# Performance work log

Measured on AMD Instinct MI355X. Metric: run time of the kernel, lower is better.

Reference implementation:

```python
import jax, jax.numpy as jnp
import numpy as np

N_NODES = 50000
N_EDGES = 1600000
IN_SIZE = 128
HIDDEN = 128
OUT_SIZE = 64
NUM_LAYERS = 3
BN_EPS = 1e-5
GIN_EPS_INIT = 1e-5


def setup_inputs() -> dict:
    key = jax.random.key(0)
    ks = jax.random.split(key, 16)
    node_feat = jax.random.normal(ks[0], (N_NODES, IN_SIZE), dtype=jnp.float32)
    src = jax.random.randint(ks[1], (N_EDGES,), 0, N_NODES)
    dst = jax.random.randint(ks[2], (N_EDGES,), 0, N_NODES)
    # per-layer MLP params (in_size == hidden, so shapes are uniform across layers)
    s1 = 1.0 / np.sqrt(IN_SIZE)
    s2 = 1.0 / np.sqrt(HIDDEN)
    W1 = jax.random.uniform(ks[3], (NUM_LAYERS, IN_SIZE, HIDDEN), jnp.float32, -s1, s1)
    b1 = jax.random.uniform(ks[4], (NUM_LAYERS, HIDDEN), jnp.float32, -s1, s1)
    gamma = jnp.ones((NUM_LAYERS, HIDDEN), jnp.float32)
    beta = jnp.zeros((NUM_LAYERS, HIDDEN), jnp.float32)
    W2 = jax.random.uniform(ks[5], (NUM_LAYERS, HIDDEN, HIDDEN), jnp.float32, -s2, s2)
    b2 = jax.random.uniform(ks[6], (NUM_LAYERS, HIDDEN), jnp.float32, -s2, s2)
    eps = jnp.full((NUM_LAYERS,), GIN_EPS_INIT, jnp.float32)  # learnable GIN eps
    Wout = jax.random.uniform(ks[7], (HIDDEN, OUT_SIZE), jnp.float32, -s2, s2)
    bout = jax.random.uniform(ks[8], (OUT_SIZE,), jnp.float32, -s2, s2)
    return {"node_feat": node_feat, "src": src, "dst": dst,
            "W1": W1, "b1": b1, "gamma": gamma, "beta": beta,
            "W2": W2, "b2": b2, "eps": eps, "Wout": Wout, "bout": bout}


def reference(node_feat, src, dst, W1, b1, gamma, beta, W2, b2, eps, Wout, bout):
    n = node_feat.shape[0]
    h = node_feat
    for i in range(NUM_LAYERS):
        # sum-aggregate source features onto destination nodes
        agg = jax.ops.segment_sum(h[src], dst, num_segments=n)  # [N, d]
        x = (1.0 + eps[i]) * h + agg
        x = x @ W1[i] + b1[i]
        # BatchNorm1d (training mode: batch statistics, biased variance)
        mu = jnp.mean(x, axis=0)
        var = jnp.var(x, axis=0)
        x = (x - mu) * jax.lax.rsqrt(var + BN_EPS) * gamma[i] + beta[i]
        x = jax.nn.relu(x)
        h = jax.nn.relu(x @ W2[i] + b2[i])
    return h @ Wout + bout
```

## Files before the change

kernel.cpp:

```cpp
#include <hip/hip_runtime.h>

#define NN 50000
#define NE 1600000
#define HID 128
#define NB 196
#define BCAP 12288
#define SLH (NN * 32)

typedef _Float16 half8 __attribute__((ext_vector_type(8)));
typedef float floatx4 __attribute__((ext_vector_type(4)));
typedef unsigned int uintx4 __attribute__((ext_vector_type(4)));

__device__ __forceinline__ void mix_acc(float a[8], half8 t) {
  uintx4 u = __builtin_bit_cast(uintx4, t);
#pragma unroll
  for (int k = 0; k < 4; ++k) {
    asm("v_fma_mix_f32 %0, %1, %2, %0 op_sel:[0,0,0] op_sel_hi:[1,0,0]"
        : "+v"(a[2 * k]) : "v"(u[k]), "v"(1.0f));
    asm("v_fma_mix_f32 %0, %1, %2, %0 op_sel:[1,0,0] op_sel_hi:[1,0,0]"
        : "+v"(a[2 * k + 1]) : "v"(u[k]), "v"(1.0f));
  }
}


#define CVT_BLK 3125
#define CNT_BLK 391

__device__ __forceinline__ void pack_one(const float* __restrict__ W1,
                                         const float* __restrict__ W2,
                                         const float* __restrict__ Wout,
                                         _Float16* __restrict__ wp, int y, int t) {
  const float* W;
  _Float16* dstp;
  int NCT;
  if (y < 3) { W = W1 + (size_t)y * 16384; dstp = wp + y * 16384; NCT = 8; }
  else if (y < 6) { W = W2 + (size_t)(y - 3) * 16384; dstp = wp + 49152 + (y - 3) * 16384; NCT = 8; }
  else { W = Wout; dstp = wp + 98304; NCT = 4; }
  if (t >= 4 * NCT * 64) return;
  int lane = t & 63;
  int ct = (t >> 6) % NCT;
  int kb = t / (64 * NCT);
  int n = ct * 16 + (lane & 15);
  int k0 = kb * 32 + (lane >> 4) * 8;
  int N = NCT * 16;
#pragma unroll
  for (int j = 0; j < 8; ++j) dstp[t * 8 + j] = (_Float16)W[(k0 + j) * N + n];
}

__global__ __launch_bounds__(256) void k_prep(
    const float* __restrict__ nf, _Float16* __restrict__ hb,
    const float* __restrict__ W1, const float* __restrict__ W2,
    const float* __restrict__ Wout, _Float16* __restrict__ wp,
    const int* __restrict__ dst, int* __restrict__ gcnt) {
  const int b = blockIdx.x;
  const int tid = threadIdx.x;
  if (b < CVT_BLK) {
    int t = b * 256 + tid;
    const float4* x4 = (const float4*)nf;
    float4 u = x4[t * 2], v = x4[t * 2 + 1];
    half8 o;
    o[0] = (_Float16)u.x; o[1] = (_Float16)u.y; o[2] = (_Float16)u.z; o[3] = (_Float16)u.w;
    o[4] = (_Float16)v.x; o[5] = (_Float16)v.y; o[6] = (_Float16)v.z; o[7] = (_Float16)v.w;
    int node = t >> 4, c = t & 15;
    ((half8*)hb)[(size_t)(c >> 2) * (NN * 4) + node * 4 + (c & 3)] = o;
  } else if (b < CVT_BLK + CNT_BLK) {
    __shared__ int cnt[NB];
    for (int i = tid; i < NB; i += 256) cnt[i] = 0;
    __syncthreads();
    int base = (b - CVT_BLK) * 4096;
    for (int i = 0; i < 16; ++i) {
      int e = base + i * 256 + tid;
      if (e < NE) atomicAdd(&cnt[dst[e] >> 8], 1);
    }
    __syncthreads();
    for (int i = tid; i < NB; i += 256)
      if (cnt[i]) atomicAdd(&gcnt[i], cnt[i]);
  } else {
    int bb = b - (CVT_BLK + CNT_BLK);
    pack_one(W1, W2, Wout, wp, bb >> 3, ((bb & 7) << 8) | tid);
  }
}


__global__ __launch_bounds__(256) void kb_basescan(const int* __restrict__ gcnt,
                                                   int* __restrict__ bbase,
                                                   int* __restrict__ bcur) {
  __shared__ int s[256];
  int tid = threadIdx.x;
  int v = (tid < NB) ? gcnt[tid] : 0;
  s[tid] = v;
  __syncthreads();
  for (int d = 1; d < 256; d <<= 1) {
    int t = (tid >= d) ? s[tid - d] : 0;
    __syncthreads();
    s[tid] += t;
    __syncthreads();
  }
  int incl = s[tid];
  if (tid < NB) {
    bbase[tid] = incl - v;
    bcur[tid] = incl - v;
  }
  if (tid == NB - 1) bbase[NB] = incl;
}

__global__ __launch_bounds__(256) void kb_partition(const int* __restrict__ src,
                                                    const int* __restrict__ dst,
                                                    int* __restrict__ bcur,
                                                    int* __restrict__ ebuf, int E) {
  __shared__ int cnt[NB];
  __shared__ int sbase[NB];
  int tid = threadIdx.x;
  for (int i = tid; i < NB; i += 256) cnt[i] = 0;
  __syncthreads();
  int base = blockIdx.x * 4096;
  int myd[16], mys[16];
#pragma unroll
  for (int i = 0; i < 16; ++i) {
    int e = base + i * 256 + tid;
    if (e < E) {
      myd[i] = dst[e];
      mys[i] = src[e];
      atomicAdd(&cnt[myd[i] >> 8], 1);
    } else {
      myd[i] = -1;
    }
  }
  __syncthreads();
  for (int i = tid; i < NB; i += 256)
    sbase[i] = cnt[i] ? atomicAdd(&bcur[i], cnt[i]) : 0;
  __syncthreads();
  for (int i = tid; i < NB; i += 256) cnt[i] = 0;
  __syncthreads();
#pragma unroll
  for (int i = 0; i < 16; ++i) {
    if (myd[i] >= 0) {
      int b = myd[i] >> 8;
      int r = atomicAdd(&cnt[b], 1);
      ebuf[sbase[b] + r] = (mys[i] << 8) | (myd[i] & 255);
    }
  }
}

__global__ __launch_bounds__(256) void kb_csr(const int* __restrict__ ebuf,
                                              const int* __restrict__ bbase,
                                              int* __restrict__ rs,
                                              unsigned short* __restrict__ eidx, int M) {
  __shared__ int cnt[256];
  __shared__ int off[256];
  __shared__ int sbuf[BCAP];
  int tid = threadIdx.x;
  int b = blockIdx.x;
  int lo = bbase[b], hi = bbase[b + 1];
  int n = hi - lo;
  cnt[tid] = 0;
  __syncthreads();
  for (int i = tid; i < n; i += 256) atomicAdd(&cnt[ebuf[lo + i] & 255], 1);
  __syncthreads();
  int v = cnt[tid];
  off[tid] = v;
  __syncthreads();
  for (int d = 1; d < 256; d <<= 1) {
    int t = (tid >= d) ? off[tid - d] : 0;
    __syncthreads();
    off[tid] += t;
    __syncthreads();
  }
  int excl = off[tid] - v;
  int gnode = b * 256 + tid;
  if (gnode < M) rs[gnode] = lo + excl;
  if (b == NB - 1 && tid == 0) rs[M] = bbase[NB];
  __syncthreads();
  cnt[tid] = excl;
  __syncthreads();
  if (n <= BCAP) {
    for (int i = tid; i < n; i += 256) {
      int ed = ebuf[lo + i];
      int r = atomicAdd(&cnt[ed & 255], 1);
      sbuf[r] = ed >> 8;
    }
    __syncthreads();
    for (int i = tid; i < n; i += 256) eidx[lo + i] = (unsigned short)sbuf[i];
  } else {
    for (int i = tid; i < n; i += 256) {
      int ed = ebuf[lo + i];
      int r = atomicAdd(&cnt[ed & 255], 1);
      eidx[lo + r] = (unsigned short)(ed >> 8);
    }
  }
}


__global__ __launch_bounds__(512, 8) void k_agg(
    const int* __restrict__ rs, const unsigned short* __restrict__ eidx,
    const float* __restrict__ eps, int layer, const _Float16* __restrict__ h,
    _Float16* __restrict__ x) {
  const int tid = threadIdx.x;
  const int b = blockIdx.x;
  const int slice = (b & 7) >> 1;
  const int tile = ((b >> 3) << 1) | (b & 1);
  const int lane = tid & 63;
  const int wid = tid >> 6;
  const int sub = lane & 3;
  const int slot = (lane >> 2) & 3;
  const int ng = lane >> 4;
  const int node = tile * 32 + wid * 4 + ng;
  const char* hbase = (const char*)(h + (size_t)slice * SLH);
  const unsigned subsh = (unsigned)sub << 4;

  float a[8] = {0.f, 0.f, 0.f, 0.f, 0.f, 0.f, 0.f, 0.f};
  int e0 = 0, e1 = 0;
  if (node < NN) {
    e0 = rs[node];
    e1 = rs[node + 1];
  }
  int e = e0 + slot;
  for (; e + 12 < e1; e += 16) {
    unsigned s0 = eidx[e];
    unsigned s1 = eidx[e + 4];
    unsigned s2 = eidx[e + 8];
    unsigned s3 = eidx[e + 12];
    half8 v0 = *(const half8*)(hbase + ((s0 << 6) | subsh));
    half8 v1 = *(const half8*)(hbase + ((s1 << 6) | subsh));
    half8 v2 = *(const half8*)(hbase + ((s2 << 6) | subsh));
    half8 v3 = *(const half8*)(hbase + ((s3 << 6) | subsh));
    half8 t01 = v0 + v1;
    half8 t23 = v2 + v3;
    mix_acc(a, t01);
    mix_acc(a, t23);
  }
  if (e + 4 < e1) {
    unsigned s0 = eidx[e];
    unsigned s1 = eidx[e + 4];
    half8 v0 = *(const half8*)(hbase + ((s0 << 6) | subsh));
    half8 v1 = *(const half8*)(hbase + ((s1 << 6) | subsh));
    half8 t01 = v0 + v1;
    mix_acc(a, t01);
    e += 8;
  }
  for (; e < e1; e += 4) {
    unsigned s0 = eidx[e];
    half8 v = *(const half8*)(hbase + ((s0 << 6) | subsh));
    mix_acc(a, v);
  }
#pragma unroll
  for (int j = 0; j < 8; ++j) {
    a[j] += __shfl_xor(a[j], 4);
    a[j] += __shfl_xor(a[j], 8);
  }
  if (slot == 0 && node < NN) {
    const float ep = 1.0f + eps[layer];
    half8 hv = *(const half8*)(hbase + (((unsigned)node << 6) | subsh));
    half8 o;
#pragma unroll
    for (int j = 0; j < 8; ++j) o[j] = (_Float16)fmaf(ep, (float)hv[j], a[j]);
    *(half8*)(x + (size_t)node * 128 + slice * 32 + sub * 8) = o;
  }
}


__global__ __launch_bounds__(1024, 8) void k_gemm1(
    const _Float16* __restrict__ wp1, const float* __restrict__ b1L,
    float* __restrict__ csum, float* __restrict__ csq, _Float16* x) {
  __shared__ _Float16 As[64 * 136];
  __shared__ float sredS[512];
  __shared__ float sredQ[512];
  const int tid = threadIdx.x;
  const int wid = tid >> 6;
  const int lane = tid & 63;
  const int slot = lane >> 4;
  const int c8 = lane & 15;
  const int c8t = tid & 15;
  const int rowBase = blockIdx.x * 64;

  {
    int row = tid >> 4;
    int gr = rowBase + row;
    half8 v = {0, 0, 0, 0, 0, 0, 0, 0};
    if (gr < NN) v = *(const half8*)(x + (size_t)gr * 128 + c8t * 8);
    *(half8*)(As + row * 136 + c8t * 8) = v;
  }
  __syncthreads();

  const int rg = wid & 3;
  const int cg = wid >> 2;
  floatx4 acc[2];
  acc[0] = (floatx4){0.f, 0.f, 0.f, 0.f};
  acc[1] = (floatx4){0.f, 0.f, 0.f, 0.f};
  const half8* wp8 = (const half8*)wp1;
#pragma unroll
  for (int kb = 0; kb < 4; ++kb) {
    half8 a = *(const half8*)(As + (rg * 16 + c8) * 136 + kb * 32 + slot * 8);
#pragma unroll
    for (int t = 0; t < 2; ++t) {
      int ct = cg * 2 + t;
      acc[t] = __builtin_amdgcn_mfma_f32_16x16x32_f16(a, wp8[(kb * 8 + ct) * 64 + lane],
                                                      acc[t], 0, 0, 0);
    }
  }
  __syncthreads();

#pragma unroll
  for (int t = 0; t < 2; ++t) {
    int ct = cg * 2 + t;
    float bv = b1L[ct * 16 + c8];
    float ps = 0.f, pq = 0.f;
#pragma unroll
    for (int reg = 0; reg < 4; ++reg) {
      int row = rg * 16 + slot * 4 + reg;
      float xv = acc[t][reg] + bv;
      As[row * 136 + ct * 16 + c8] = (_Float16)xv;
      if (rowBase + row < NN) {
        ps += xv;
        pq += xv * xv;
      }
    }
    ps += __shfl_xor(ps, 16);
    ps += __shfl_xor(ps, 32);
    pq += __shfl_xor(pq, 16);
    pq += __shfl_xor(pq, 32);
    if (lane < 16) {
      sredS[wid * 32 + t * 16 + lane] = ps;
      sredQ[wid * 32 + t * 16 + lane] = pq;
    }
  }
  __syncthreads();

  {
    int row = tid >> 4;
    int gr = rowBase + row;
    if (gr < NN) {
      half8 v = *(half8*)(As + row * 136 + c8t * 8);
      *(half8*)(x + (size_t)gr * 128 + c8t * 8) = v;
    }
  }
  if (tid < 128) {
    int c = tid;
    int wbase = (c >> 5) * 4;
    int loc = c & 31;
    float s = sredS[wbase * 32 + loc] + sredS[(wbase + 1) * 32 + loc] +
              sredS[(wbase + 2) * 32 + loc] + sredS[(wbase + 3) * 32 + loc];
    atomicAdd(&csum[c], s);
  } else if (tid < 256) {
    int c = tid - 128;
    int wbase = (c >> 5) * 4;
    int loc = c & 31;
    float q = sredQ[wbase * 32 + loc] + sredQ[(wbase + 1) * 32 + loc] +
              sredQ[(wbase + 2) * 32 + loc] + sredQ[(wbase + 3) * 32 + loc];
    atomicAdd(&csq[c], q);
  }
}


template <int FINAL>
__global__ __launch_bounds__(1024, 8) void k_bn_gemm2(
    const _Float16* __restrict__ x, const _Float16* __restrict__ wp2,
    const float* __restrict__ b2L, const float* __restrict__ gammaL,
    const float* __restrict__ betaL, const float* __restrict__ csum,
    const float* __restrict__ csq, _Float16* __restrict__ hout,
    const _Float16* __restrict__ wpo, const float* __restrict__ boutp,
    float* __restrict__ out) {
  __shared__ _Float16 As[64 * 136];
  const int tid = threadIdx.x;
  const int wid = tid >> 6;
  const int lane = tid & 63;
  const int slot = lane >> 4;
  const int c8 = lane & 15;
  const int c8t = tid & 15;
  const int rowBase = blockIdx.x * 64;

  float sc[8], sh[8];
  {
    const float invM = 1.0f / (float)NN;
#pragma unroll
    for (int j = 0; j < 8; ++j) {
      int k = c8t * 8 + j;
      float mu = csum[k] * invM;
      float var = csq[k] * invM - mu * mu;
      float g = gammaL[k] * rsqrtf(var + 1e-5f);
      sc[j] = g;
      sh[j] = fmaf(-mu, g, betaL[k]);
    }
  }
  {
    int row = tid >> 4;
    int gr = rowBase + row;
    half8 v = {0, 0, 0, 0, 0, 0, 0, 0};
    if (gr < NN) {
      v = *(const half8*)(x + (size_t)gr * 128 + c8t * 8);
#pragma unroll
      for (int j = 0; j < 8; ++j)
        v[j] = (_Float16)fmaxf(fmaf((float)v[j], sc[j], sh[j]), 0.f);
    }
    *(half8*)(As + row * 136 + c8t * 8) = v;
  }
  __syncthreads();

  const int rg = wid & 3;
  const int cg = wid >> 2;
  floatx4 acc[2];
  acc[0] = (floatx4){0.f, 0.f, 0.f, 0.f};
  acc[1] = (floatx4){0.f, 0.f, 0.f, 0.f};
  const half8* wp8 = (const half8*)wp2;
#pragma unroll
  for (int kb = 0; kb < 4; ++kb) {
    half8 a = *(const half8*)(As + (rg * 16 + c8) * 136 + kb * 32 + slot * 8);
#pragma unroll
    for (int t = 0; t < 2; ++t) {
      int ct = cg * 2 + t;
      acc[t] = __builtin_amdgcn_mfma_f32_16x16x32_f16(a, wp8[(kb * 8 + ct) * 64 + lane],
                                                      acc[t], 0, 0, 0);
    }
  }
  __syncthreads();
#pragma unroll
  for (int t = 0; t < 2; ++t) {
    int ct = cg * 2 + t;
    float bv = b2L[ct * 16 + c8];
#pragma unroll
    for (int reg = 0; reg < 4; ++reg) {
      int row = rg * 16 + slot * 4 + reg;
      As[row * 136 + ct * 16 + c8] = (_Float16)fmaxf(acc[t][reg] + bv, 0.f);
    }
  }
  __syncthreads();

  if (FINAL == 0) {
    int row = tid >> 4;
    int gr = rowBase + row;
    if (gr < NN) {
      half8 v = *(half8*)(As + row * 136 + c8t * 8);
      *(half8*)(hout + (size_t)(c8t >> 2) * SLH + (size_t)gr * 32 + (c8t & 3) * 8) = v;
    }
  } else {
    if (cg < 2) {
      floatx4 acc3[2];
      acc3[0] = (floatx4){0.f, 0.f, 0.f, 0.f};
      acc3[1] = (floatx4){0.f, 0.f, 0.f, 0.f};
      const half8* wo8 = (const half8*)wpo;
#pragma unroll
      for (int kb = 0; kb < 4; ++kb) {
        half8 a = *(const half8*)(As + (rg * 16 + c8) * 136 + kb * 32 + slot * 8);
#pragma unroll
        for (int t = 0; t < 2; ++t) {
          int ct = cg * 2 + t;
          acc3[t] = __builtin_amdgcn_mfma_f32_16x16x32_f16(
              a, wo8[(kb * 4 + ct) * 64 + lane], acc3[t], 0, 0, 0);
        }
      }
#pragma unroll
      for (int t = 0; t < 2; ++t) {
        int ct = cg * 2 + t;
        float bv = boutp[ct * 16 + c8];
#pragma unroll
        for (int reg = 0; reg < 4; ++reg) {
          int gr = rowBase + rg * 16 + slot * 4 + reg;
          if (gr < NN) out[(size_t)gr * 64 + ct * 16 + c8] = acc3[t][reg] + bv;
        }
      }
    }
  }
}


extern "C" void kernel_launch(void* const* d_in, const int* in_sizes, int n_in,
                              void* d_out, int out_size, void* d_ws, size_t ws_size,
                              hipStream_t stream) {
  const float* node_feat = (const float*)d_in[0];
  const int* src = (const int*)d_in[1];
  const int* dst = (const int*)d_in[2];
  const float* W1 = (const float*)d_in[3];
  const float* b1 = (const float*)d_in[4];
  const float* gamma = (const float*)d_in[5];
  const float* beta = (const float*)d_in[6];
  const float* W2 = (const float*)d_in[7];
  const float* b2 = (const float*)d_in[8];
  const float* eps = (const float*)d_in[9];
  const float* Wout = (const float*)d_in[10];
  const float* bout = (const float*)d_in[11];
  float* out = (float*)d_out;

  int* rs = (int*)d_ws;
  int* gcnt = rs + 50176;
  int* bbase = gcnt + 256;
  int* bcur = bbase + 256;
  float* stats = (float*)(bcur + 256);
  int* eidx = (int*)(stats + 768);
  _Float16* hb = (_Float16*)(eidx + NE);
  _Float16* xb = hb + (size_t)NN * HID;
  _Float16* wp = xb + (size_t)NN * HID;
  int* ebuf = (int*)(wp + 106496);

  unsigned short* eidx16 = (unsigned short*)eidx;

  hipMemsetAsync(gcnt, 0, (256 * 3 + 768) * sizeof(int), stream);

  k_prep<<<CVT_BLK + CNT_BLK + 56, 256, 0, stream>>>(node_feat, hb, W1, W2, Wout,
                                                     wp, dst, gcnt);
  kb_basescan<<<1, 256, 0, stream>>>(gcnt, bbase, bcur);
  kb_partition<<<CNT_BLK, 256, 0, stream>>>(src, dst, bcur, ebuf, NE);
  kb_csr<<<NB, 256, 0, stream>>>(ebuf, bbase, rs, eidx16, NN);

  const int rowTiles = (NN + 63) / 64;
  const int aggBlocks = 1564 * 4;

  for (int L = 0; L < 3; ++L) {
    float* csum = stats + L * 256;
    float* csq = csum + 128;
    k_agg<<<aggBlocks, 512, 0, stream>>>(rs, eidx16, eps, L, hb, xb);
    k_gemm1<<<rowTiles, 1024, 0, stream>>>(wp + (size_t)L * 16384,
                                           b1 + (size_t)L * HID, csum, csq, xb);
    if (L < 2) {
      k_bn_gemm2<0><<<rowTiles, 1024, 0, stream>>>(
          xb, wp + 49152 + (size_t)L * 16384, b2 + (size_t)L * HID,
          gamma + (size_t)L * HID, beta + (size_t)L * HID, csum, csq, hb,
          nullptr, nullptr, nullptr);
    } else {
      k_bn_gemm2<1><<<rowTiles, 1024, 0, stream>>>(
          xb, wp + 49152 + (size_t)L * 16384, b2 + (size_t)L * HID,
          gamma + (size_t)L * HID, beta + (size_t)L * HID, csum, csq, nullptr,
          wp + 98304, bout, out);
    }
  }
}
```

Baseline: 394.0 us.

## Recompute GEMM1 in BN kernel instead of writing pre-BN activations back

GEMM1 is split into a stats-only kernel that computes x@W1+b1 per 16-row wave tile and accumulates per-channel sum and sum-of-squares without storing the result. The next kernel recomputes GEMM1 from the aggregated input, applies the folded BN scale and shift (with b1 folded into the shift) and ReLU, then runs GEMM2. This removes one full write and one read of the 50000x128 fp16 intermediate per layer, paid for by doing GEMM1 twice. Block-level shared atomics cut the number of global atomics.

Result: faster. 382.3 us (-3.0%).

```diff
diff --git a/kernel.cpp b/kernel.cpp
--- a/kernel.cpp
+++ b/kernel.cpp
@@ -259,102 +259,68 @@
 }
 
 
-__global__ __launch_bounds__(1024, 8) void k_gemm1(
-    const _Float16* __restrict__ wp1, const float* __restrict__ b1L,
-    float* __restrict__ csum, float* __restrict__ csq, _Float16* x) {
-  __shared__ _Float16 As[64 * 136];
-  __shared__ float sredS[512];
-  __shared__ float sredQ[512];
+__global__ __launch_bounds__(512, 8) void k_stats(
+    const _Float16* __restrict__ x, const _Float16* __restrict__ wp1,
+    const float* __restrict__ b1L, float* __restrict__ csum,
+    float* __restrict__ csq) {
+  __shared__ float sS[128];
+  __shared__ float sQ[128];
   const int tid = threadIdx.x;
   const int wid = tid >> 6;
   const int lane = tid & 63;
   const int slot = lane >> 4;
   const int c8 = lane & 15;
-  const int c8t = tid & 15;
-  const int rowBase = blockIdx.x * 64;
-
-  {
-    int row = tid >> 4;
-    int gr = rowBase + row;
-    half8 v = {0, 0, 0, 0, 0, 0, 0, 0};
-    if (gr < NN) v = *(const half8*)(x + (size_t)gr * 128 + c8t * 8);
-    *(half8*)(As + row * 136 + c8t * 8) = v;
-  }
-  __syncthreads();
-
-  const int rg = wid & 3;
-  const int cg = wid >> 2;
-  floatx4 acc[2];
-  acc[0] = (floatx4){0.f, 0.f, 0.f, 0.f};
-  acc[1] = (floatx4){0.f, 0.f, 0.f, 0.f};
-  const half8* wp8 = (const half8*)wp1;
-#pragma unroll
-  for (int kb = 0; kb < 4; ++kb) {
-    half8 a = *(const half8*)(As + (rg * 16 + c8) * 136 + kb * 32 + slot * 8);
-#pragma unroll
-    for (int t = 0; t < 2; ++t) {
-      int ct = cg * 2 + t;
-      acc[t] = __builtin_amdgcn_mfma_f32_16x16x32_f16(a, wp8[(kb * 8 + ct) * 64 + lane],
-                                                      acc[t], 0, 0, 0);
-    }
-  }
-  __syncthreads();
-
-#pragma unroll
-  for (int t = 0; t < 2; ++t) {
-    int ct = cg * 2 + t;
-    float bv = b1L[ct * 16 + c8];
-    float ps = 0.f, pq = 0.f;
-#pragma unroll
-    for (int reg = 0; reg < 4; ++reg) {
-      int row = rg * 16 + slot * 4 + reg;
-      float xv = acc[t][reg] + bv;
-      As[row * 136 + ct * 16 + c8] = (_Float16)xv;
-      if (rowBase + row < NN) {
+  if (tid < 128) { sS[tid] = 0.f; sQ[tid] = 0.f; }
+  __syncthreads();
+  const int s = blockIdx.x * 8 + wid;
+  if (s < 3125) {
+    const int rowBase = s * 16;
+    half8 af[4];
+#pragma unroll
+    for (int kb = 0; kb < 4; ++kb)
+      af[kb] = *(const half8*)(x + (size_t)(rowBase + c8) * 128 + kb * 32 + slot * 8);
+    const half8* wp8 = (const half8*)wp1;
+    float pS[8], pQ[8];
+#pragma unroll
+    for (int ct = 0; ct < 8; ++ct) {
+      floatx4 acc = (floatx4){0.f, 0.f, 0.f, 0.f};
+#pragma unroll
+      for (int kb = 0; kb < 4; ++kb)
+        acc = __builtin_amdgcn_mfma_f32_16x16x32_f16(af[kb], wp8[(kb * 8 + ct) * 64 + lane],
+                                                     acc, 0, 0, 0);
+      float bv = b1L[ct * 16 + c8];
+      float ps = 0.f, pq = 0.f;
+#pragma unroll
+      for (int reg = 0; reg < 4; ++reg) {
+        float xv = acc[reg] + bv;
         ps += xv;
         pq += xv * xv;
       }
-    }
-    ps += __shfl_xor(ps, 16);
-    ps += __shfl_xor(ps, 32);
-    pq += __shfl_xor(pq, 16);
-    pq += __shfl_xor(pq, 32);
+      ps += __shfl_xor(ps, 16);
+      ps += __shfl_xor(ps, 32);
+      pq += __shfl_xor(pq, 16);
+      pq += __shfl_xor(pq, 32);
+      pS[ct] = ps;
+      pQ[ct] = pq;
+    }
     if (lane < 16) {
-      sredS[wid * 32 + t * 16 + lane] = ps;
-      sredQ[wid * 32 + t * 16 + lane] = pq;
-    }
-  }
-  __syncthreads();
-
-  {
-    int row = tid >> 4;
-    int gr = rowBase + row;
-    if (gr < NN) {
-      half8 v = *(half8*)(As + row * 136 + c8t * 8);
-      *(half8*)(x + (size_t)gr * 128 + c8t * 8) = v;
-    }
-  }
-  if (tid < 128) {
-    int c = tid;
-    int wbase = (c >> 5) * 4;
-    int loc = c & 31;
-    float s = sredS[wbase * 32 + loc] + sredS[(wbase + 1) * 32 + loc] +
-              sredS[(wbase + 2) * 32 + loc] + sredS[(wbase + 3) * 32 + loc];
-    atomicAdd(&csum[c], s);
-  } else if (tid < 256) {
-    int c = tid - 128;
-    int wbase = (c >> 5) * 4;
-    int loc = c & 31;
-    float q = sredQ[wbase * 32 + loc] + sredQ[(wbase + 1) * 32 + loc] +
-              sredQ[(wbase + 2) * 32 + loc] + sredQ[(wbase + 3) * 32 + loc];
-    atomicAdd(&csq[c], q);
-  }
+#pragma unroll
+      for (int ct = 0; ct < 8; ++ct) {
+        atomicAdd(&sS[ct * 16 + c8], pS[ct]);
+        atomicAdd(&sQ[ct * 16 + c8], pQ[ct]);
+      }
+    }
+  }
+  __syncthreads();
+  if (tid < 128) atomicAdd(&csum[tid], sS[tid]);
+  else if (tid < 256) atomicAdd(&csq[tid - 128], sQ[tid - 128]);
 }
 
 
 template <int FINAL>
-__global__ __launch_bounds__(1024, 8) void k_bn_gemm2(
-    const _Float16* __restrict__ x, const _Float16* __restrict__ wp2,
+__global__ __launch_bounds__(1024, 8) void k_bngemm12(
+    const _Float16* __restrict__ x, const _Float16* __restrict__ wp1,
+    const float* __restrict__ b1L, const _Float16* __restrict__ wp2,
     const float* __restrict__ b2L, const float* __restrict__ gammaL,
     const float* __restrict__ betaL, const float* __restrict__ csum,
     const float* __restrict__ csq, _Float16* __restrict__ hout,
@@ -368,48 +334,73 @@
   const int c8 = lane & 15;
   const int c8t = tid & 15;
   const int rowBase = blockIdx.x * 64;
-
-  float sc[8], sh[8];
+  const int rg = wid & 3;
+  const int cg = wid >> 2;
+
+  float sc_t[2], sh_t[2];
   {
     const float invM = 1.0f / (float)NN;
 #pragma unroll
-    for (int j = 0; j < 8; ++j) {
-      int k = c8t * 8 + j;
+    for (int t = 0; t < 2; ++t) {
+      int k = (cg * 2 + t) * 16 + c8;
       float mu = csum[k] * invM;
       float var = csq[k] * invM - mu * mu;
       float g = gammaL[k] * rsqrtf(var + 1e-5f);
-      sc[j] = g;
-      sh[j] = fmaf(-mu, g, betaL[k]);
+      sc_t[t] = g;
+      sh_t[t] = fmaf(b1L[k] - mu, g, betaL[k]);
     }
   }
   {
     int row = tid >> 4;
     int gr = rowBase + row;
     half8 v = {0, 0, 0, 0, 0, 0, 0, 0};
-    if (gr < NN) {
-      v = *(const half8*)(x + (size_t)gr * 128 + c8t * 8);
-#pragma unroll
-      for (int j = 0; j < 8; ++j)
-        v[j] = (_Float16)fmaxf(fmaf((float)v[j], sc[j], sh[j]), 0.f);
-    }
+    if (gr < NN) v = *(const half8*)(x + (size_t)gr * 128 + c8t * 8);
     *(half8*)(As + row * 136 + c8t * 8) = v;
   }
   __syncthreads();
 
-  const int rg = wid & 3;
-  const int cg = wid >> 2;
   floatx4 acc[2];
   acc[0] = (floatx4){0.f, 0.f, 0.f, 0.f};
   acc[1] = (floatx4){0.f, 0.f, 0.f, 0.f};
-  const half8* wp8 = (const half8*)wp2;
-#pragma unroll
-  for (int kb = 0; kb < 4; ++kb) {
-    half8 a = *(const half8*)(As + (rg * 16 + c8) * 136 + kb * 32 + slot * 8);
-#pragma unroll
-    for (int t = 0; t < 2; ++t) {
-      int ct = cg * 2 + t;
-      acc[t] = __builtin_amdgcn_mfma_f32_16x16x32_f16(a, wp8[(kb * 8 + ct) * 64 + lane],
-                                                      acc[t], 0, 0, 0);
+  {
+    const half8* wp8 = (const half8*)wp1;
+#pragma unroll
+    for (int kb = 0; kb < 4; ++kb) {
+      half8 a = *(const half8*)(As + (rg * 16 + c8) * 136 + kb * 32 + slot * 8);
+#pragma unroll
+      for (int t = 0; t < 2; ++t) {
+        int ct = cg * 2 + t;
+        acc[t] = __builtin_amdgcn_mfma_f32_16x16x32_f16(a, wp8[(kb * 8 + ct) * 64 + lane],
+                                                        acc[t], 0, 0, 0);
+      }
+    }
+  }
+  __syncthreads();
+#pragma unroll
+  for (int t = 0; t < 2; ++t) {
+    int ct = cg * 2 + t;
+#pragma unroll
+    for (int reg = 0; reg < 4; ++reg) {
+      int row = rg * 16 + slot * 4 + reg;
+      As[row * 136 + ct * 16 + c8] =
+          (_Float16)fmaxf(fmaf(acc[t][reg], sc_t[t], sh_t[t]), 0.f);
+    }
+  }
+  __syncthreads();
+
+  acc[0] = (floatx4){0.f, 0.f, 0.f, 0.f};
+  acc[1] = (floatx4){0.f, 0.f, 0.f, 0.f};
+  {
+    const half8* wp8 = (const half8*)wp2;
+#pragma unroll
+    for (int kb = 0; kb < 4; ++kb) {
+      half8 a = *(const half8*)(As + (rg * 16 + c8) * 136 + kb * 32 + slot * 8);
+#pragma unroll
+      for (int t = 0; t < 2; ++t) {
+        int ct = cg * 2 + t;
+        acc[t] = __builtin_amdgcn_mfma_f32_16x16x32_f16(a, wp8[(kb * 8 + ct) * 64 + lane],
+                                                        acc[t], 0, 0, 0);
+      }
     }
   }
   __syncthreads();
@@ -508,16 +499,18 @@
     float* csum = stats + L * 256;
     float* csq = csum + 128;
     k_agg<<<aggBlocks, 512, 0, stream>>>(rs, eidx16, eps, L, hb, xb);
-    k_gemm1<<<rowTiles, 1024, 0, stream>>>(wp + (size_t)L * 16384,
-                                           b1 + (size_t)L * HID, csum, csq, xb);
+    k_stats<<<391, 512, 0, stream>>>(xb, wp + (size_t)L * 16384,
+                                     b1 + (size_t)L * HID, csum, csq);
     if (L < 2) {
-      k_bn_gemm2<0><<<rowTiles, 1024, 0, stream>>>(
-          xb, wp + 49152 + (size_t)L * 16384, b2 + (size_t)L * HID,
+      k_bngemm12<0><<<rowTiles, 1024, 0, stream>>>(
+          xb, wp + (size_t)L * 16384, b1 + (size_t)L * HID,
+          wp + 49152 + (size_t)L * 16384, b2 + (size_t)L * HID,
           gamma + (size_t)L * HID, beta + (size_t)L * HID, csum, csq, hb,
           nullptr, nullptr, nullptr);
     } else {
-      k_bn_gemm2<1><<<rowTiles, 1024, 0, stream>>>(
-          xb, wp + 49152 + (size_t)L * 16384, b2 + (size_t)L * HID,
+      k_bngemm12<1><<<rowTiles, 1024, 0, stream>>>(
+          xb, wp + (size_t)L * 16384, b1 + (size_t)L * HID,
+          wp + 49152 + (size_t)L * 16384, b2 + (size_t)L * HID,
           gamma + (size_t)L * HID, beta + (size_t)L * HID, csum, csq, nullptr,
           wp + 98304, bout, out);
     }
```
